# Optimization experiments

Measured on AMD Instinct MI355X. Metric: run time of the kernel, lower is better.

Reference implementation:

```python
import jax, jax.numpy as jnp
import numpy as np
from functools import partial

B, H, W, C = 16, 64, 64, 512      # images, feature H, feature W, channels
R = 256                            # raw RPN proposals per image (sorted by objectness)
N_REGIONS = 64                     # regions kept after NMS
PH, PW = 7, 7                      # pool_size (h, w)
IOU_THR = 0.4
FH, FW = H, W                      # feature_size (h, w)
NEG = -jnp.inf


def _nms_indices(roi):
    # roi: [R, 4] (x, y, w, h). Scores are descending by construction
    # (tf.reverse(tf.range(n)/n)), so greedy NMS processes rows in order.
    x, y, w, h = roi[:, 0], roi[:, 1], roi[:, 2], roi[:, 3]
    y1, x1, y2, x2 = y, x, y + h, x + w
    area = (y2 - y1) * (x2 - x1)
    ih = jnp.maximum(jnp.minimum(y2[:, None], y2[None, :]) - jnp.maximum(y1[:, None], y1[None, :]), 0.0)
    iw = jnp.maximum(jnp.minimum(x2[:, None], x2[None, :]) - jnp.maximum(x1[:, None], x1[None, :]), 0.0)
    inter = ih * iw
    union = area[:, None] + area[None, :] - inter
    iou = jnp.where(union > 0, inter / union, 0.0)  # [R, R]

    def step(keep, xs):
        i, row = xs
        suppressed = jnp.any(keep & (row > IOU_THR))
        return keep.at[i].set(~suppressed), None

    keep, _ = jax.lax.scan(step, jnp.zeros((R,), bool), (jnp.arange(R), iou))
    rank = jnp.cumsum(keep.astype(jnp.int32)) - 1
    valid = keep & (rank < N_REGIONS)
    # Unfilled slot j gets tail index R - N_REGIONS + j, which is exactly
    # tf.concat([nms, tf.range(n_roi)[size(nms) - n_regions:]], 0).
    fill = R - N_REGIONS + jnp.arange(N_REGIONS)
    idx = fill.at[jnp.where(valid, rank, N_REGIONS)].set(jnp.arange(R), mode='drop')
    return idx


def _fix_axis(mn, mx, ps, fs):
    pad = ps - (mx - mn)
    fix_min = mn < pad // 2
    fix_max = fs - mx < (1 + pad) // 2
    symmetric = (pad > 0) & ~(fix_min | fix_max)
    omin = jnp.where(symmetric, mn - pad // 2, mn)
    omax = jnp.where(symmetric, mx + (1 + pad) // 2, mx)
    omin = jnp.where((pad > 0) & fix_min, 0, omin)
    omax = jnp.where((pad > 0) & fix_min, ps, omax)
    omin = jnp.where((pad > 0) & fix_max, fs - ps, omin)
    omax = jnp.where((pad > 0) & fix_max, fs, omax)
    return omin, omax


def _clip_roi(roi):
    # roi: [B, N_REGIONS, 4] float (x, y, w, h) -> int32 clipped (x, y, w, h)
    x_min = jnp.maximum(0.0, roi[..., 0]).astype(jnp.int32)
    y_min = jnp.maximum(0.0, roi[..., 1]).astype(jnp.int32)
    x_max = jnp.minimum(float(FW), roi[..., 0] + roi[..., 2]).astype(jnp.int32)
    y_max = jnp.minimum(float(FH), roi[..., 1] + roi[..., 3]).astype(jnp.int32)
    x_min, x_max = _fix_axis(x_min, x_max, PW, FW)   # x axis uses si=1 (width)
    y_min, y_max = _fix_axis(y_min, y_max, PH, FH)   # y axis uses si=0 (height)
    return jnp.stack([x_min, y_min, x_max - x_min, y_max - y_min], axis=-1)


def _pool_one(fm, r):
    # fm: [H, W, C]; r: int32 (x, y, w, h).
    # Faithful to the traced tf.function behaviour of _pool_roi: region.shape[0]
    # is dynamic (None) so region_shape = pool_size, hence h_step = w_step = 1:
    # bins i < PH-1 are single rows y+i; the last bin spans rows [y+PH-1, y+h).
    x, y, w, h = r[0], r[1], r[2], r[3]
    ii = y + jnp.arange(PH - 1)
    jj = x + jnp.arange(PW - 1)
    rmask = (jnp.arange(H) >= y + PH - 1) & (jnp.arange(H) < y + h)
    cmask = (jnp.arange(W) >= x + PW - 1) & (jnp.arange(W) < x + w)
    block = fm[ii[:, None], jj[None, :], :]                                   # [PH-1, PW-1, C]
    col_strip = jnp.max(jnp.where(cmask[None, :, None], fm, NEG), axis=1)     # [H, C]
    corner = jnp.max(jnp.where(rmask[:, None], col_strip, NEG), axis=0)       # [C]
    row_strip = jnp.max(jnp.where(rmask[:, None, None], fm[:, jj, :], NEG), axis=0)  # [PW-1, C]
    top = jnp.concatenate([block, col_strip[ii][:, None, :]], axis=1)         # [PH-1, PW, C]
    bottom = jnp.concatenate([row_strip, corner[None, :]], axis=0)[None]      # [1, PW, C]
    return jnp.concatenate([top, bottom], axis=0)                             # [PH, PW, C]


def _forward(features, roi):
    idx = jax.vmap(_nms_indices)(roi)                           # [B, N_REGIONS]
    roi_nms = jnp.take_along_axis(roi, idx[..., None], axis=1)  # [B, N_REGIONS, 4]
    roi_clipped = _clip_roi(roi_nms)                            # int32 [B, N_REGIONS, 4]
    pooled = jax.vmap(lambda fm, rs: jax.vmap(partial(_pool_one, fm))(rs))(features, roi_clipped)
    return pooled, roi_clipped


def setup_inputs():
    key = jax.random.key(0)
    k1, k2, k3 = jax.random.split(key, 3)
    features = jax.random.normal(k1, (B, H, W, C), dtype=jnp.float32)
    xy = jax.random.uniform(k2, (B, R, 2), dtype=jnp.float32) * 60.0
    wh = jax.random.uniform(k3, (B, R, 2), dtype=jnp.float32) * 30.0 + 2.0
    roi = jnp.concatenate([xy, wh], axis=-1)
    return {"features": features, "roi": roi}


def reference(features, roi):
    return _forward(features, roi)
```

## Files before the change

### kernel.cpp

```cpp
#include <hip/hip_runtime.h>
#include <math.h>

namespace {
constexpr int kB = 16, kH = 64, kW = 64, kC = 512;
constexpr int kR = 256, kN = 64, kPH = 7, kPW = 7;
constexpr int kC4 = kC / 4;
constexpr float kIouThr = 0.4f;
constexpr size_t kPooledElems = (size_t)kB * kN * kPH * kPW * kC;
}

__device__ __forceinline__ float4 max4(float4 a, float4 b) {
    return make_float4(fmaxf(a.x, b.x), fmaxf(a.y, b.y),
                       fmaxf(a.z, b.z), fmaxf(a.w, b.w));
}

__global__ __launch_bounds__(256) void nms_clip_kernel(
        const float* __restrict__ roi, float* __restrict__ out_roi) {
    const int b = blockIdx.x;
    const int tid = threadIdx.x;
    const float* r = roi + (size_t)b * kR * 4;

    __shared__ float4 box[kR];
    __shared__ float area[kR];
    __shared__ unsigned long long M[kR][4];
    __shared__ unsigned long long kw[4];
    __shared__ int idx[kN];

    if (tid < kN) idx[tid] = kR - kN + tid;

    const float4 rr = ((const float4*)r)[tid];
    const float x1 = rr.x, y1 = rr.y, x2 = rr.x + rr.z, y2 = rr.y + rr.w;
    box[tid] = make_float4(x1, y1, x2, y2);
    area[tid] = (y2 - y1) * (x2 - x1);
    __syncthreads();

    {
        unsigned long long m0 = 0, m1 = 0, m2 = 0, m3 = 0;
        const float ai = area[tid];
        for (int j = 0; j < kR; ++j) {
            const float4 bj = box[j];
            const float ih = fmaxf(fminf(y2, bj.w) - fmaxf(y1, bj.y), 0.0f);
            const float iw = fmaxf(fminf(x2, bj.z) - fmaxf(x1, bj.x), 0.0f);
            const float inter = ih * iw;
            const float uni = ai + area[j] - inter;
            const float iou = (uni > 0.0f) ? (inter / uni) : 0.0f;
            if (iou > kIouThr) {
                const unsigned long long bit = 1ull << (j & 63);
                if ((j >> 6) == 0) m0 |= bit;
                else if ((j >> 6) == 1) m1 |= bit;
                else if ((j >> 6) == 2) m2 |= bit;
                else m3 |= bit;
            }
        }
        M[tid][0] = m0; M[tid][1] = m1; M[tid][2] = m2; M[tid][3] = m3;
    }
    __syncthreads();

    if (tid == 0) {
        unsigned long long s0 = 0, s1 = 0, s2 = 0, s3 = 0;
        unsigned long long k0 = 0, k1 = 0, k2 = 0, k3 = 0;
        unsigned long long n0 = M[0][0], n1 = M[0][1], n2 = M[0][2], n3 = M[0][3];
#pragma unroll
        for (int wi = 0; wi < 4; ++wi) {
            for (int bi = 0; bi < 64; ++bi) {
                const unsigned long long m0 = n0, m1 = n1, m2 = n2, m3 = n3;
                const int ip = (wi * 64 + bi + 1) & 255;
                n0 = M[ip][0]; n1 = M[ip][1]; n2 = M[ip][2]; n3 = M[ip][3];
                const unsigned long long sw =
                    (wi == 0) ? s0 : (wi == 1) ? s1 : (wi == 2) ? s2 : s3;
                if (!((sw >> bi) & 1ull)) {
                    const unsigned long long bit = 1ull << bi;
                    if (wi == 0) k0 |= bit;
                    else if (wi == 1) k1 |= bit;
                    else if (wi == 2) k2 |= bit;
                    else k3 |= bit;
                    s0 |= m0; s1 |= m1; s2 |= m2; s3 |= m3;
                }
            }
        }
        kw[0] = k0; kw[1] = k1; kw[2] = k2; kw[3] = k3;
    }
    __syncthreads();

    {
        const int wi = tid >> 6, bi = tid & 63;
        const unsigned long long kwv = kw[wi];
        if ((kwv >> bi) & 1ull) {
            int rank = 0;
            for (int w2 = 0; w2 < wi; ++w2) rank += __popcll(kw[w2]);
            const unsigned long long below =
                (bi == 0) ? 0ull : (~0ull >> (64 - bi));
            rank += __popcll(kwv & below);
            if (rank < kN) idx[rank] = tid;
        }
    }
    __syncthreads();

    if (tid < kN) {
        const int i = idx[tid];
        const float x = r[i * 4 + 0], y = r[i * 4 + 1];
        const float w = r[i * 4 + 2], h = r[i * 4 + 3];
        int x_min = (int)fmaxf(0.0f, x);
        int y_min = (int)fmaxf(0.0f, y);
        int x_max = (int)fminf((float)kW, x + w);
        int y_max = (int)fminf((float)kH, y + h);
        {
            const int pad = kPW - (x_max - x_min);
            const bool fmn = x_min < (pad >> 1);
            const bool fmx = (kW - x_max) < ((1 + pad) >> 1);
            const bool sym = (pad > 0) && !(fmn || fmx);
            int omin = sym ? (x_min - (pad >> 1)) : x_min;
            int omax = sym ? (x_max + ((1 + pad) >> 1)) : x_max;
            if ((pad > 0) && fmn) { omin = 0; omax = kPW; }
            if ((pad > 0) && fmx) { omin = kW - kPW; omax = kW; }
            x_min = omin; x_max = omax;
        }
        {
            const int pad = kPH - (y_max - y_min);
            const bool fmn = y_min < (pad >> 1);
            const bool fmx = (kH - y_max) < ((1 + pad) >> 1);
            const bool sym = (pad > 0) && !(fmn || fmx);
            int omin = sym ? (y_min - (pad >> 1)) : y_min;
            int omax = sym ? (y_max + ((1 + pad) >> 1)) : y_max;
            if ((pad > 0) && fmn) { omin = 0; omax = kPH; }
            if ((pad > 0) && fmx) { omin = kH - kPH; omax = kH; }
            y_min = omin; y_max = omax;
        }
        float4 rf;
        rf.x = (float)x_min; rf.y = (float)y_min;
        rf.z = (float)(x_max - x_min); rf.w = (float)(y_max - y_min);
        ((float4*)out_roi)[b * kN + tid] = rf;
    }
}

__global__ __launch_bounds__(512) void pool_kernel(
        const float4* __restrict__ fm4, const float4* __restrict__ rcf,
        float4* __restrict__ out4) {
    constexpr int kNBlk = kB * kN;
    constexpr int kCpx = kNBlk / 8;
    const int rid = (blockIdx.x & 7) * kCpx + (blockIdx.x >> 3);
    const int b = rid >> 6;
    const int tid = threadIdx.x;
    const int s = tid >> 7;
    const int t = tid & 127;

    const float4 rf = rcf[rid];
    const int x = (int)rf.x, y = (int)rf.y;
    const int w = (int)rf.z, h = (int)rf.w;

    const float4* fm = fm4 + (size_t)b * kH * kW * kC4 + t;
    float4* out = out4 + (size_t)rid * (kPH * kPW) * kC4 + t;

    const float NI = -__builtin_inff();
    const float4 ninf = make_float4(NI, NI, NI, NI);

    for (int p = s; p < 6; p += 4) {
        const float4* row = fm + ((y + p) * kW + x) * kC4;
        float4 v0 = row[0 * kC4], v1 = row[1 * kC4], v2 = row[2 * kC4];
        float4 v3 = row[3 * kC4], v4 = row[4 * kC4], v5 = row[5 * kC4];
        out[(p * 7 + 0) * kC4] = v0;
        out[(p * 7 + 1) * kC4] = v1;
        out[(p * 7 + 2) * kC4] = v2;
        out[(p * 7 + 3) * kC4] = v3;
        out[(p * 7 + 4) * kC4] = v4;
        out[(p * 7 + 5) * kC4] = v5;
        float4 m0 = ninf, m1 = ninf, m2 = ninf, m3 = ninf;
        int j = 6;
        for (; j + 4 <= w; j += 4) {
            float4 a0 = row[(j + 0) * kC4], a1 = row[(j + 1) * kC4];
            float4 a2 = row[(j + 2) * kC4], a3 = row[(j + 3) * kC4];
            m0 = max4(m0, a0); m1 = max4(m1, a1);
            m2 = max4(m2, a2); m3 = max4(m3, a3);
        }
        for (; j < w; ++j) m0 = max4(m0, row[j * kC4]);
        out[(p * 7 + 6) * kC4] = max4(max4(m0, m1), max4(m2, m3));
    }

    float4 pm[7];
#pragma unroll
    for (int o = 0; o < 7; ++o) pm[o] = ninf;
    for (int i = y + 6 + s; i < y + h; i += 4) {
        const float4* row = fm + (i * kW + x) * kC4;
#pragma unroll
        for (int q = 0; q < 6; ++q) pm[q] = max4(pm[q], row[q * kC4]);
        float4 c0 = pm[6], c1 = ninf, c2 = ninf, c3 = ninf;
        int j = 6;
        for (; j + 4 <= w; j += 4) {
            float4 a0 = row[(j + 0) * kC4], a1 = row[(j + 1) * kC4];
            float4 a2 = row[(j + 2) * kC4], a3 = row[(j + 3) * kC4];
            c0 = max4(c0, a0); c1 = max4(c1, a1);
            c2 = max4(c2, a2); c3 = max4(c3, a3);
        }
        for (; j < w; ++j) c0 = max4(c0, row[j * kC4]);
        pm[6] = max4(max4(c0, c1), max4(c2, c3));
    }

    __shared__ float4 red[kPH][kC4];
    if (s == 1) {
#pragma unroll
        for (int o = 0; o < 7; ++o) red[o][t] = pm[o];
    }
    __syncthreads();
    if (s == 2) {
#pragma unroll
        for (int o = 0; o < 7; ++o) red[o][t] = max4(red[o][t], pm[o]);
    }
    __syncthreads();
    if (s == 3) {
#pragma unroll
        for (int o = 0; o < 7; ++o) red[o][t] = max4(red[o][t], pm[o]);
    }
    __syncthreads();
    if (s == 0) {
#pragma unroll
        for (int o = 0; o < 7; ++o) {
            out[(42 + o) * kC4] = max4(pm[o], red[o][t]);
        }
    }
}

extern "C" void kernel_launch(void* const* d_in, const int* in_sizes, int n_in,
                              void* d_out, int out_size, void* d_ws, size_t ws_size,
                              hipStream_t stream) {
    (void)in_sizes; (void)n_in; (void)d_ws; (void)ws_size; (void)out_size;
    const float* features = (const float*)d_in[0];
    const float* roi = (const float*)d_in[1];
    float* out = (float*)d_out;
    float* out_roi = out + kPooledElems;

    nms_clip_kernel<<<kB, 256, 0, stream>>>(roi, out_roi);
    pool_kernel<<<kB * kN, 512, 0, stream>>>(
        (const float4*)features, (const float4*)out_roi, (float4*)out);
}
```

Measured before the change: 312.3 us.

## Split pooling work per region into channel quarters with eight row slices

The pool kernel now launches four blocks per region, each covering 32 float4 channel groups with 256 threads arranged as 8 row slices instead of 4. The first six rows are each handled by their own slice, and the partial maxima are combined through a tree reduction in shared memory. The aim is more blocks and more parallelism along rows, so long ROIs spend less time in serial row loops and the GPU is better filled. In exchange there are more barriers, smaller per-wave 512-byte contiguous accesses, and the ROI header is read four times per region.

Measured after the change: 307.3 us. No clear change (-1.6%).

```diff
diff --git a/kernel.cpp b/kernel.cpp
--- a/kernel.cpp
+++ b/kernel.cpp
@@ -133,28 +133,32 @@
     }
 }
 
-__global__ __launch_bounds__(512) void pool_kernel(
+__global__ __launch_bounds__(256) void pool_kernel(
         const float4* __restrict__ fm4, const float4* __restrict__ rcf,
         float4* __restrict__ out4) {
-    constexpr int kNBlk = kB * kN;
+    constexpr int kNBlk = kB * kN * 4;
     constexpr int kCpx = kNBlk / 8;
-    const int rid = (blockIdx.x & 7) * kCpx + (blockIdx.x >> 3);
+    const int bid = (blockIdx.x & 7) * kCpx + (blockIdx.x >> 3);
+    const int rid = bid >> 2;
+    const int q4 = bid & 3;
     const int b = rid >> 6;
     const int tid = threadIdx.x;
-    const int s = tid >> 7;
-    const int t = tid & 127;
+    const int s = tid >> 5;
+    const int t = tid & 31;
+    const int g = q4 * 32 + t;
 
     const float4 rf = rcf[rid];
     const int x = (int)rf.x, y = (int)rf.y;
     const int w = (int)rf.z, h = (int)rf.w;
 
-    const float4* fm = fm4 + (size_t)b * kH * kW * kC4 + t;
-    float4* out = out4 + (size_t)rid * (kPH * kPW) * kC4 + t;
+    const float4* fm = fm4 + (size_t)b * kH * kW * kC4 + g;
+    float4* out = out4 + (size_t)rid * (kPH * kPW) * kC4 + g;
 
     const float NI = -__builtin_inff();
     const float4 ninf = make_float4(NI, NI, NI, NI);
 
-    for (int p = s; p < 6; p += 4) {
+    if (s < 6) {
+        const int p = s;
         const float4* row = fm + ((y + p) * kW + x) * kC4;
         float4 v0 = row[0 * kC4], v1 = row[1 * kC4], v2 = row[2 * kC4];
         float4 v3 = row[3 * kC4], v4 = row[4 * kC4], v5 = row[5 * kC4];
@@ -179,7 +183,7 @@
     float4 pm[7];
 #pragma unroll
     for (int o = 0; o < 7; ++o) pm[o] = ninf;
-    for (int i = y + 6 + s; i < y + h; i += 4) {
+    for (int i = y + 6 + s; i < y + h; i += 8) {
         const float4* row = fm + (i * kW + x) * kC4;
 #pragma unroll
         for (int q = 0; q < 6; ++q) pm[q] = max4(pm[q], row[q * kC4]);
@@ -195,26 +199,36 @@
         pm[6] = max4(max4(c0, c1), max4(c2, c3));
     }
 
-    __shared__ float4 red[kPH][kC4];
+    __shared__ float4 red[4][kPH][32];
+    if (s >= 4) {
+#pragma unroll
+        for (int o = 0; o < 7; ++o) red[s - 4][o][t] = pm[o];
+    }
+    __syncthreads();
+    if (s < 4) {
+#pragma unroll
+        for (int o = 0; o < 7; ++o) pm[o] = max4(pm[o], red[s][o][t]);
+    }
+    __syncthreads();
+    if (s == 2 || s == 3) {
+#pragma unroll
+        for (int o = 0; o < 7; ++o) red[s - 2][o][t] = pm[o];
+    }
+    __syncthreads();
+    if (s < 2) {
+#pragma unroll
+        for (int o = 0; o < 7; ++o) pm[o] = max4(pm[o], red[s][o][t]);
+    }
+    __syncthreads();
     if (s == 1) {
 #pragma unroll
-        for (int o = 0; o < 7; ++o) red[o][t] = pm[o];
-    }
-    __syncthreads();
-    if (s == 2) {
-#pragma unroll
-        for (int o = 0; o < 7; ++o) red[o][t] = max4(red[o][t], pm[o]);
-    }
-    __syncthreads();
-    if (s == 3) {
-#pragma unroll
-        for (int o = 0; o < 7; ++o) red[o][t] = max4(red[o][t], pm[o]);
+        for (int o = 0; o < 7; ++o) red[0][o][t] = pm[o];
     }
     __syncthreads();
     if (s == 0) {
 #pragma unroll
         for (int o = 0; o < 7; ++o) {
-            out[(42 + o) * kC4] = max4(pm[o], red[o][t]);
+            out[(42 + o) * kC4] = max4(pm[o], red[0][o][t]);
         }
     }
 }
@@ -229,6 +243,6 @@
     float* out_roi = out + kPooledElems;
 
     nms_clip_kernel<<<kB, 256, 0, stream>>>(roi, out_roi);
-    pool_kernel<<<kB * kN, 512, 0, stream>>>(
+    pool_kernel<<<kB * kN * 4, 256, 0, stream>>>(
         (const float4*)features, (const float4*)out_roi, (float4*)out);
 }
```
